# Performance work log

Hardware: AMD Instinct MI355X
Metric: run time of the kernel (lower is better)

## Reference

```python
import jax, jax.numpy as jnp
import numpy as np

Q, S, D = 8192, 30, 512
THRESH = 30


def setup_inputs() -> dict:
    key = jax.random.key(0)
    ks = jax.random.split(key, 8)
    return {
        "query_encode": jax.random.normal(ks[0], (Q, D), jnp.float32),
        "support_encode": jax.random.normal(ks[1], (S, D), jnp.float32),
        # binary CTR-style labels in {0,1}
        "support_y": jnp.round(jax.random.uniform(ks[2], (1, S), jnp.float32)),
        "support_predict": jax.random.normal(ks[3], (S,), jnp.float32),
        "query_predict": jax.random.normal(ks[4], (Q,), jnp.float32),
        "fc1_w": jax.random.normal(ks[5], (D,), jnp.float32) / np.sqrt(D),
        "fc1_b": jnp.zeros((), jnp.float32),
        # AdjustLayer params: scale init 6, bias init 0, shape [THRESH, 1]
        "adjust_scale": jnp.full((THRESH, 1), 6.0, jnp.float32),
        "adjust_bias": jnp.zeros((THRESH, 1), jnp.float32),
        "num_samples": S,
    }


def reference(query_encode, support_encode, support_y, support_predict,
              query_predict, fc1_w, fc1_b, adjust_scale, adjust_bias,
              num_samples):
    # Pairwise L1 distance: [Q, S, D]
    distance = jnp.abs(query_encode[:, None, :] - support_encode[None, :, :])
    # Linear scorer over feature dim -> [Q, S]
    similar_score = jnp.einsum("qsd,d->qs", distance, fc1_w) + fc1_b
    attn = jax.nn.softmax(similar_score, axis=1)  # softmax over support dim
    # Residual of support labels vs predictor output: [1, S]
    delta_y = support_y - jax.nn.sigmoid(support_predict)[None, :]
    delta_y_hat = jnp.sum(delta_y * attn, axis=1)  # [Q]
    # AdjustLayer: indexed scale/bias (index is a static int here)
    scale = jnp.abs(adjust_scale[num_samples - 1, 0])
    bias = adjust_bias[num_samples - 1, 0]
    prediction = delta_y_hat * scale + bias + query_predict  # [Q]
    # Mean L2 distance to support set: [Q]
    mean_l2 = jnp.mean(jnp.sqrt(jnp.sum(distance ** 2, axis=-1)), axis=-1)
    return prediction, mean_l2
```

## Files before the change

kernel.cpp:

```cpp
#include <hip/hip_runtime.h>
#include <math.h>


#define QN 8192
#define SN 30
#define DN 512
#define BLK 512
#define QT 16
#define SCHUNK 10
#define NPASS 3
#define SROW 580
#define PRW 17
#define PSTR 31

__global__ __launch_bounds__(BLK, 2)
void resus_one(const float* __restrict__ query,
               const float* __restrict__ support,
               const float* __restrict__ support_y,
               const float* __restrict__ support_pr,
               const float* __restrict__ query_pr,
               const float* __restrict__ fc1_w,
               const float* __restrict__ adj_scale,
               const float* __restrict__ adj_bias,
               const int*   __restrict__ num_samples,
               float* __restrict__ out)
{
    __shared__ float  sp[SCHUNK * SROW];
    __shared__ float  praw_sc[SCHUNK * QT * PRW];
    __shared__ float  praw_sq[SCHUNK * QT * PRW];
    __shared__ float2 part[QT * PSTR];

    const int tid   = threadIdx.x;
    const int ql    = tid & 15;
    const int dseg  = (tid >> 4) & 15;
    const int shalf = tid >> 8;
    const int q     = blockIdx.x * QT + ql;

    const float* qp = query + (size_t)q * DN + dseg * 32;
    float4 q0 = *reinterpret_cast<const float4*>(qp +  0);
    float4 q1 = *reinterpret_cast<const float4*>(qp +  4);
    float4 q2 = *reinterpret_cast<const float4*>(qp +  8);
    float4 q3 = *reinterpret_cast<const float4*>(qp + 12);
    float4 q4 = *reinterpret_cast<const float4*>(qp + 16);
    float4 q5 = *reinterpret_cast<const float4*>(qp + 20);
    float4 q6 = *reinterpret_cast<const float4*>(qp + 24);
    float4 q7 = *reinterpret_cast<const float4*>(qp + 28);
    const float* wp = fc1_w + dseg * 32;
    float4 w0 = *reinterpret_cast<const float4*>(wp +  0);
    float4 w1 = *reinterpret_cast<const float4*>(wp +  4);
    float4 w2 = *reinterpret_cast<const float4*>(wp +  8);
    float4 w3 = *reinterpret_cast<const float4*>(wp + 12);
    float4 w4 = *reinterpret_cast<const float4*>(wp + 16);
    float4 w5 = *reinterpret_cast<const float4*>(wp + 20);
    float4 w6 = *reinterpret_cast<const float4*>(wp + 24);
    float4 w7 = *reinterpret_cast<const float4*>(wp + 28);

#define PIN4(V) asm volatile("" : "+v"((V).x), "+v"((V).y), "+v"((V).z), "+v"((V).w))
    PIN4(q0); PIN4(q1); PIN4(q2); PIN4(q3);
    PIN4(q4); PIN4(q5); PIN4(q6); PIN4(q7);
    PIN4(w0); PIN4(w1); PIN4(w2); PIN4(w3);
    PIN4(w4); PIN4(w5); PIN4(w6); PIN4(w7);
#undef PIN4

#define ACC4(QV, WV, SV) { float d_; \
    d_ = (QV).x - (SV).x; sc = fmaf((WV).x, fabsf(d_), sc); sq = fmaf(d_, d_, sq); \
    d_ = (QV).y - (SV).y; sc = fmaf((WV).y, fabsf(d_), sc); sq = fmaf(d_, d_, sq); \
    d_ = (QV).z - (SV).z; sc = fmaf((WV).z, fabsf(d_), sc); sq = fmaf(d_, d_, sq); \
    d_ = (QV).w - (SV).w; sc = fmaf((WV).w, fabsf(d_), sc); sq = fmaf(d_, d_, sq); }

    const int sbase = dseg * 36;
    const int pbase = ql * PRW + dseg;
    const int sl0   = shalf * (SCHUNK / 2);

    for (int pass = 0; pass < NPASS; ++pass) {
        __syncthreads();

        const float4* sg = reinterpret_cast<const float4*>(
            support + (size_t)pass * SCHUNK * DN);
        for (int i = tid; i < SCHUNK * 128; i += BLK) {
            const int row = i >> 7, c4 = i & 127;
            *reinterpret_cast<float4*>(
                sp + row * SROW + 36 * (c4 >> 3) + 4 * (c4 & 7)) = sg[i];
        }
        __syncthreads();

#pragma unroll
        for (int k = 0; k < SCHUNK / 2; ++k) {
            const int sl = sl0 + k;
            const float* sr = sp + sl * SROW + sbase;
            const float4 s0 = *reinterpret_cast<const float4*>(sr +  0);
            const float4 s1 = *reinterpret_cast<const float4*>(sr +  4);
            const float4 s2 = *reinterpret_cast<const float4*>(sr +  8);
            const float4 s3 = *reinterpret_cast<const float4*>(sr + 12);
            const float4 s4 = *reinterpret_cast<const float4*>(sr + 16);
            const float4 s5 = *reinterpret_cast<const float4*>(sr + 20);
            const float4 s6 = *reinterpret_cast<const float4*>(sr + 24);
            const float4 s7 = *reinterpret_cast<const float4*>(sr + 28);

            float sc = 0.0f, sq = 0.0f;
            ACC4(q0, w0, s0) ACC4(q1, w1, s1)
            ACC4(q2, w2, s2) ACC4(q3, w3, s3)
            ACC4(q4, w4, s4) ACC4(q5, w5, s5)
            ACC4(q6, w6, s6) ACC4(q7, w7, s7)

            praw_sc[sl * (QT * PRW) + pbase] = sc;
            praw_sq[sl * (QT * PRW) + pbase] = sq;
        }
        __syncthreads();

        if (tid < SCHUNK * QT) {
            const int sl = tid >> 4, qq = tid & 15;
            const int b = sl * (QT * PRW) + qq * PRW;
            float sc = 0.0f, sq = 0.0f;
#pragma unroll
            for (int d = 0; d < 16; ++d) {
                sc += praw_sc[b + d];
                sq += praw_sq[b + d];
            }
            part[qq * PSTR + pass * SCHUNK + sl] = make_float2(sc, sq);
        }
    }
#undef ACC4
    __syncthreads();

    const int grp  = tid >> 5;
    const int s32  = tid & 31;
    const bool valid = (s32 < SN);
    const int  si  = valid ? s32 : 0;

    float dy = 0.0f;
    if (valid)
        dy = support_y[s32] - 1.0f / (1.0f + expf(-support_pr[s32]));

    const int ns = num_samples[0];
    const float ascale = fabsf(adj_scale[ns - 1]);
    const float abias  = adj_bias[ns - 1];

    const int qg = blockIdx.x * QT + grp;
    const float2 pr = part[grp * PSTR + si];

    float scv = valid ? pr.x : -1e30f;
    float ssv = valid ? pr.y : 0.0f;

    float m = scv;
#pragma unroll
    for (int off = 16; off >= 1; off >>= 1)
        m = fmaxf(m, __shfl_xor(m, off));

    float e   = valid ? expf(scv - m) : 0.0f;
    float den = e;
    float num = dy * e;
    float l2  = valid ? sqrtf(ssv) : 0.0f;
#pragma unroll
    for (int off = 16; off >= 1; off >>= 1) {
        den += __shfl_xor(den, off);
        num += __shfl_xor(num, off);
        l2  += __shfl_xor(l2,  off);
    }

    if (s32 == 0) {
        out[qg]      = num / den * ascale + abias + query_pr[qg];
        out[QN + qg] = l2 * (1.0f / (float)SN);
    }
}

extern "C" void kernel_launch(void* const* d_in, const int* in_sizes, int n_in,
                              void* d_out, int out_size, void* d_ws, size_t ws_size,
                              hipStream_t stream)
{
    const float* query      = (const float*)d_in[0];
    const float* support    = (const float*)d_in[1];
    const float* support_y  = (const float*)d_in[2];
    const float* support_pr = (const float*)d_in[3];
    const float* query_pr   = (const float*)d_in[4];
    const float* fc1_w      = (const float*)d_in[5];
    const float* adj_scale  = (const float*)d_in[7];
    const float* adj_bias   = (const float*)d_in[8];
    const int*   num_s      = (const int*)d_in[9];
    float* out = (float*)d_out;

    dim3 grid(QN / QT);
    hipLaunchKernelGGL(resus_one, grid, dim3(BLK), 0, stream,
                       query, support, support_y, support_pr, query_pr,
                       fc1_w, adj_scale, adj_bias, num_s, out);
}
```

Baseline: 93.27 us.

## Process two queries per thread to double support reuse from LDS

```diff
diff --git a/kernel.cpp b/kernel.cpp
--- a/kernel.cpp
+++ b/kernel.cpp
@@ -6,7 +6,7 @@
 #define SN 30
 #define DN 512
 #define BLK 512
-#define QT 16
+#define QT 32
 #define SCHUNK 10
 #define NPASS 3
 #define SROW 580
@@ -34,17 +34,27 @@
     const int ql    = tid & 15;
     const int dseg  = (tid >> 4) & 15;
     const int shalf = tid >> 8;
-    const int q     = blockIdx.x * QT + ql;
-
-    const float* qp = query + (size_t)q * DN + dseg * 32;
-    float4 q0 = *reinterpret_cast<const float4*>(qp +  0);
-    float4 q1 = *reinterpret_cast<const float4*>(qp +  4);
-    float4 q2 = *reinterpret_cast<const float4*>(qp +  8);
-    float4 q3 = *reinterpret_cast<const float4*>(qp + 12);
-    float4 q4 = *reinterpret_cast<const float4*>(qp + 16);
-    float4 q5 = *reinterpret_cast<const float4*>(qp + 20);
-    float4 q6 = *reinterpret_cast<const float4*>(qp + 24);
-    float4 q7 = *reinterpret_cast<const float4*>(qp + 28);
+    const int qA    = blockIdx.x * QT + ql;
+    const int qB    = qA + 16;
+
+    const float* qpA = query + (size_t)qA * DN + dseg * 32;
+    float4 a0 = *reinterpret_cast<const float4*>(qpA +  0);
+    float4 a1 = *reinterpret_cast<const float4*>(qpA +  4);
+    float4 a2 = *reinterpret_cast<const float4*>(qpA +  8);
+    float4 a3 = *reinterpret_cast<const float4*>(qpA + 12);
+    float4 a4 = *reinterpret_cast<const float4*>(qpA + 16);
+    float4 a5 = *reinterpret_cast<const float4*>(qpA + 20);
+    float4 a6 = *reinterpret_cast<const float4*>(qpA + 24);
+    float4 a7 = *reinterpret_cast<const float4*>(qpA + 28);
+    const float* qpB = query + (size_t)qB * DN + dseg * 32;
+    float4 b0 = *reinterpret_cast<const float4*>(qpB +  0);
+    float4 b1 = *reinterpret_cast<const float4*>(qpB +  4);
+    float4 b2 = *reinterpret_cast<const float4*>(qpB +  8);
+    float4 b3 = *reinterpret_cast<const float4*>(qpB + 12);
+    float4 b4 = *reinterpret_cast<const float4*>(qpB + 16);
+    float4 b5 = *reinterpret_cast<const float4*>(qpB + 20);
+    float4 b6 = *reinterpret_cast<const float4*>(qpB + 24);
+    float4 b7 = *reinterpret_cast<const float4*>(qpB + 28);
     const float* wp = fc1_w + dseg * 32;
     float4 w0 = *reinterpret_cast<const float4*>(wp +  0);
     float4 w1 = *reinterpret_cast<const float4*>(wp +  4);
@@ -56,21 +66,32 @@
     float4 w7 = *reinterpret_cast<const float4*>(wp + 28);
 
 #define PIN4(V) asm volatile("" : "+v"((V).x), "+v"((V).y), "+v"((V).z), "+v"((V).w))
-    PIN4(q0); PIN4(q1); PIN4(q2); PIN4(q3);
-    PIN4(q4); PIN4(q5); PIN4(q6); PIN4(q7);
+    PIN4(a0); PIN4(a1); PIN4(a2); PIN4(a3);
+    PIN4(a4); PIN4(a5); PIN4(a6); PIN4(a7);
+    PIN4(b0); PIN4(b1); PIN4(b2); PIN4(b3);
+    PIN4(b4); PIN4(b5); PIN4(b6); PIN4(b7);
     PIN4(w0); PIN4(w1); PIN4(w2); PIN4(w3);
     PIN4(w4); PIN4(w5); PIN4(w6); PIN4(w7);
 #undef PIN4
 
-#define ACC4(QV, WV, SV) { float d_; \
-    d_ = (QV).x - (SV).x; sc = fmaf((WV).x, fabsf(d_), sc); sq = fmaf(d_, d_, sq); \
-    d_ = (QV).y - (SV).y; sc = fmaf((WV).y, fabsf(d_), sc); sq = fmaf(d_, d_, sq); \
-    d_ = (QV).z - (SV).z; sc = fmaf((WV).z, fabsf(d_), sc); sq = fmaf(d_, d_, sq); \
-    d_ = (QV).w - (SV).w; sc = fmaf((WV).w, fabsf(d_), sc); sq = fmaf(d_, d_, sq); }
-
-    const int sbase = dseg * 36;
-    const int pbase = ql * PRW + dseg;
-    const int sl0   = shalf * (SCHUNK / 2);
+#define ACC2(QA, QB, WV, SV) { float dA_, dB_; \
+    dA_ = (QA).x - (SV).x; dB_ = (QB).x - (SV).x; \
+    scA = fmaf((WV).x, fabsf(dA_), scA); sqA = fmaf(dA_, dA_, sqA); \
+    scB = fmaf((WV).x, fabsf(dB_), scB); sqB = fmaf(dB_, dB_, sqB); \
+    dA_ = (QA).y - (SV).y; dB_ = (QB).y - (SV).y; \
+    scA = fmaf((WV).y, fabsf(dA_), scA); sqA = fmaf(dA_, dA_, sqA); \
+    scB = fmaf((WV).y, fabsf(dB_), scB); sqB = fmaf(dB_, dB_, sqB); \
+    dA_ = (QA).z - (SV).z; dB_ = (QB).z - (SV).z; \
+    scA = fmaf((WV).z, fabsf(dA_), scA); sqA = fmaf(dA_, dA_, sqA); \
+    scB = fmaf((WV).z, fabsf(dB_), scB); sqB = fmaf(dB_, dB_, sqB); \
+    dA_ = (QA).w - (SV).w; dB_ = (QB).w - (SV).w; \
+    scA = fmaf((WV).w, fabsf(dA_), scA); sqA = fmaf(dA_, dA_, sqA); \
+    scB = fmaf((WV).w, fabsf(dB_), scB); sqB = fmaf(dB_, dB_, sqB); }
+
+    const int sbase  = dseg * 36;
+    const int pbaseA = ql * PRW + dseg;
+    const int pbaseB = (ql + 16) * PRW + dseg;
+    const int sl0    = shalf * (SCHUNK / 2);
 
     for (int pass = 0; pass < NPASS; ++pass) {
         __syncthreads();
@@ -97,19 +118,21 @@
             const float4 s6 = *reinterpret_cast<const float4*>(sr + 24);
             const float4 s7 = *reinterpret_cast<const float4*>(sr + 28);
 
-            float sc = 0.0f, sq = 0.0f;
-            ACC4(q0, w0, s0) ACC4(q1, w1, s1)
-            ACC4(q2, w2, s2) ACC4(q3, w3, s3)
-            ACC4(q4, w4, s4) ACC4(q5, w5, s5)
-            ACC4(q6, w6, s6) ACC4(q7, w7, s7)
-
-            praw_sc[sl * (QT * PRW) + pbase] = sc;
-            praw_sq[sl * (QT * PRW) + pbase] = sq;
+            float scA = 0.0f, sqA = 0.0f, scB = 0.0f, sqB = 0.0f;
+            ACC2(a0, b0, w0, s0) ACC2(a1, b1, w1, s1)
+            ACC2(a2, b2, w2, s2) ACC2(a3, b3, w3, s3)
+            ACC2(a4, b4, w4, s4) ACC2(a5, b5, w5, s5)
+            ACC2(a6, b6, w6, s6) ACC2(a7, b7, w7, s7)
+
+            praw_sc[sl * (QT * PRW) + pbaseA] = scA;
+            praw_sq[sl * (QT * PRW) + pbaseA] = sqA;
+            praw_sc[sl * (QT * PRW) + pbaseB] = scB;
+            praw_sq[sl * (QT * PRW) + pbaseB] = sqB;
         }
         __syncthreads();
 
         if (tid < SCHUNK * QT) {
-            const int sl = tid >> 4, qq = tid & 15;
+            const int sl = tid >> 5, qq = tid & 31;
             const int b = sl * (QT * PRW) + qq * PRW;
             float sc = 0.0f, sq = 0.0f;
 #pragma unroll
@@ -120,45 +143,50 @@
             part[qq * PSTR + pass * SCHUNK + sl] = make_float2(sc, sq);
         }
     }
-#undef ACC4
+#undef ACC2
     __syncthreads();
 
-    const int grp  = tid >> 5;
-    const int s32  = tid & 31;
-    const bool valid = (s32 < SN);
-    const int  si  = valid ? s32 : 0;
-
-    float dy = 0.0f;
-    if (valid)
-        dy = support_y[s32] - 1.0f / (1.0f + expf(-support_pr[s32]));
+    const int grp = tid >> 4;
+    const int sA  = tid & 15;
+    const int sB  = sA + 16;
+    const bool vB = (sB < SN);
+
+    const float dyA = support_y[sA] - 1.0f / (1.0f + expf(-support_pr[sA]));
+    float dyB = 0.0f;
+    if (vB)
+        dyB = support_y[sB] - 1.0f / (1.0f + expf(-support_pr[sB]));
 
     const int ns = num_samples[0];
     const float ascale = fabsf(adj_scale[ns - 1]);
     const float abias  = adj_bias[ns - 1];
 
     const int qg = blockIdx.x * QT + grp;
-    const float2 pr = part[grp * PSTR + si];
-
-    float scv = valid ? pr.x : -1e30f;
-    float ssv = valid ? pr.y : 0.0f;
-
-    float m = scv;
-#pragma unroll
-    for (int off = 16; off >= 1; off >>= 1)
+    const float2 prA = part[grp * PSTR + sA];
+    const float2 prB = part[grp * PSTR + (vB ? sB : 0)];
+
+    const float scvA = prA.x;
+    const float ssvA = prA.y;
+    const float scvB = vB ? prB.x : -1e30f;
+    const float ssvB = vB ? prB.y : 0.0f;
+
+    float m = fmaxf(scvA, scvB);
+#pragma unroll
+    for (int off = 8; off >= 1; off >>= 1)
         m = fmaxf(m, __shfl_xor(m, off));
 
-    float e   = valid ? expf(scv - m) : 0.0f;
-    float den = e;
-    float num = dy * e;
-    float l2  = valid ? sqrtf(ssv) : 0.0f;
-#pragma unroll
-    for (int off = 16; off >= 1; off >>= 1) {
+    const float eA = expf(scvA - m);
+    const float eB = vB ? expf(scvB - m) : 0.0f;
+    float den = eA + eB;
+    float num = __fadd_rn(__fmul_rn(dyA, eA), __fmul_rn(dyB, eB));
+    float l2  = sqrtf(ssvA) + (vB ? sqrtf(ssvB) : 0.0f);
+#pragma unroll
+    for (int off = 8; off >= 1; off >>= 1) {
         den += __shfl_xor(den, off);
         num += __shfl_xor(num, off);
         l2  += __shfl_xor(l2,  off);
     }
 
-    if (s32 == 0) {
+    if (sA == 0) {
         out[qg]      = num / den * ascale + abias + query_pr[qg];
         out[QN + qg] = l2 * (1.0f / (float)SN);
     }
```

Result: no change. 94.41 us (+1.2%).
